# Optimization experiments

Hardware: AMD Instinct MI355X
Metric: run time of the kernel (lower is better)

## Reference

```python
import jax, jax.numpy as jnp
import numpy as np

# hyperparams (match CombinedPeakLoss defaults)
ALPHA, BETA, GAMMA, DELTA, EPSILON = 1.0, 2.0, 1.0, 0.5, 0.5
PEAK_WINDOW = 2
DAYTIME_WEIGHT = 2.0
TEMPERATURE = 0.1
HOURS = 24
NEG = -1e9


def setup_inputs() -> dict:
    key = jax.random.key(0)
    k1, k2 = jax.random.split(key)
    B, S = 16384, 720  # 30 days of hourly data
    y_pred = jax.random.uniform(k1, (B, S), dtype=jnp.float32)
    y_true = jax.random.uniform(k2, (B, S), dtype=jnp.float32)
    return {"y_pred": y_pred, "y_true": y_true}


def _soft_peaks(y_bdh, day_mask, hours):
    # y_bdh: [B,D,H]; day_mask: [1,D,H] bool; hours: [H]
    masked = jnp.where(day_mask, y_bdh, NEG)
    attn = jax.nn.softmax(masked / TEMPERATURE, axis=-1)  # [B,D,H]
    peak_val = (attn * y_bdh).sum(-1)                      # [B,D]
    peak_time = (attn * hours).sum(-1)                     # [B,D]
    return peak_val, peak_time


def reference(y_pred, y_true):
    B, S = y_true.shape
    D = S // HOURS
    dt = y_true.dtype

    # default is_daytime: tiled hour-of-day, daytime = 6..20 inclusive
    t = jnp.tile(jnp.arange(HOURS), D)[:S]                 # [S]
    is_day = ((t >= 6) & (t <= 20))                        # [S] bool
    day_mask = is_day.reshape(1, D, HOURS)                 # [1,D,H]
    hours = jnp.arange(HOURS, dtype=dt)                    # [H]

    yt = y_true.reshape(B, D, HOURS)
    yp = y_pred.reshape(B, D, HOURS)

    # L_overall
    L_overall = jnp.mean((y_pred - y_true) ** 2)

    # soft peak extraction for both true and pred
    t_pv, t_pt = _soft_peaks(yt, day_mask, hours)
    p_pv, p_pt = _soft_peaks(yp, day_mask, hours)
    L_peak_value = jnp.mean((p_pv - t_pv) ** 2)
    L_peak_time = jnp.mean((p_pt - t_pt) ** 2)

    # peak shape loss: hard argmax on daytime-masked truth, windowed normalized MSE
    masked_true = jnp.where(day_mask, yt, NEG)
    peak_idx = jnp.argmax(masked_true, axis=-1)            # [B,D]
    ws = jnp.maximum(0, peak_idx - PEAK_WINDOW)            # [B,D]
    we = jnp.minimum(HOURS, peak_idx + PEAK_WINDOW + 1)    # [B,D]
    h = jnp.arange(HOURS)
    wmask = (h[None, None, :] >= ws[..., None]) & (h[None, None, :] < we[..., None])  # [B,D,H]
    tmax = jnp.max(jnp.where(wmask, yt, NEG), axis=-1)     # [B,D]
    pmax = jnp.max(jnp.where(wmask, yp, NEG), axis=-1)     # [B,D]
    valid = tmax > 1e-6
    tmax_safe = jnp.where(valid, tmax, 1.0)
    diff = yp / (pmax[..., None] + 1e-6) - yt / tmax_safe[..., None]
    wlen = (we - ws).astype(dt)
    mse_win = jnp.sum(jnp.where(wmask, diff ** 2, 0.0), axis=-1) / wlen  # [B,D]
    L_peak_shape = jnp.sum(jnp.where(valid, mse_win, 0.0)) / (jnp.sum(valid) + 1e-6)

    # daytime-weighted extra MSE
    dw = jnp.where(is_day, DAYTIME_WEIGHT, 1.0).astype(dt)  # [S]
    weighted_mse = jnp.mean((y_pred - y_true) ** 2 * dw)
    L_daytime = weighted_mse - L_overall

    total = (ALPHA * L_overall + BETA * L_peak_value + GAMMA * L_peak_time
             + DELTA * L_peak_shape + EPSILON * L_daytime)
    return total
```

## Files before the change

### kernel.cpp

```cpp
#include <hip/hip_runtime.h>
#include <hip/hip_fp16.h>

#define HOURS 24
#define RPB 256
#define PSTR 25


__global__ __launch_bounds__(256, 6) void peakloss_main(
    const float* __restrict__ ypred, const float* __restrict__ ytrue,
    float* __restrict__ partials, int nrows, int nblocks) {
  __shared__ __half2 ltp[RPB * PSTR];

  const int tid = threadIdx.x;
  const int tile0 = blockIdx.x * RPB;
  const int rows = min(RPB, nrows - tile0);

  float s_sq = 0.f, s_day = 0.f, s_pv = 0.f, s_pt = 0.f, s_shape = 0.f, s_valid = 0.f;

  if (rows == RPB) {
    const float4* t4 = (const float4*)(ytrue + (size_t)tile0 * HOURS);
    const float4* p4 = (const float4*)(ypred + (size_t)tile0 * HOURS);
#pragma unroll
    for (int j = 0; j < 6; ++j) {
      int f4 = tid + j * 256;
      float4 a = t4[f4];
      float4 b = p4[f4];
      int pa0 = f4 * 4 + f4 / 6;
      ltp[pa0 + 0] = __floats2half2_rn(a.x, b.x);
      ltp[pa0 + 1] = __floats2half2_rn(a.y, b.y);
      ltp[pa0 + 2] = __floats2half2_rn(a.z, b.z);
      ltp[pa0 + 3] = __floats2half2_rn(a.w, b.w);
      int h0 = 4 * (f4 % 6);
      float dx = b.x - a.x, dy = b.y - a.y, dz = b.z - a.z, dw = b.w - a.w;
      float qx = dx * dx, qy = dy * dy, qz = dz * dz, qw = dw * dw;
      s_sq += qx + qy + qz + qw;
      s_day += ((h0 + 0 >= 6) & (h0 + 0 <= 20)) ? qx : 0.f;
      s_day += ((h0 + 1 >= 6) & (h0 + 1 <= 20)) ? qy : 0.f;
      s_day += ((h0 + 2 >= 6) & (h0 + 2 <= 20)) ? qz : 0.f;
      s_day += ((h0 + 3 >= 6) & (h0 + 3 <= 20)) ? qw : 0.f;
    }
  } else {
    for (int d = tid; d < rows * HOURS; d += 256) {
      float tv = ytrue[(size_t)tile0 * HOURS + d];
      float pv = ypred[(size_t)tile0 * HOURS + d];
      int pa = d + d / HOURS;
      ltp[pa] = __floats2half2_rn(tv, pv);
      float dd = (pv - tv) * (pv - tv);
      int h = d % HOURS;
      s_sq += dd;
      s_day += ((h >= 6) & (h <= 20)) ? dd : 0.f;
    }
  }
  __syncthreads();

  if (tid < rows) {
    const __half2* row = ltp + tid * PSTR;

    float mt = -1e30f, mp = -1e30f;
    int idx = 6;
#pragma unroll
    for (int h = 6; h <= 20; ++h) {
      __half2 v = row[h];
      float th = __low2float(v), ph = __high2float(v);
      if (th > mt) { mt = th; idx = h; }
      mp = fmaxf(mp, ph);
    }

    int ws = idx - 2;
    float den_t = 0.f, nv_t = 0.f, nt_t = 0.f;
    float den_p = 0.f, nv_p = 0.f, nt_p = 0.f;
    float tmax = -1e30f, pmax = -1e30f;
    float St2 = 0.f, Sp2 = 0.f, Stp = 0.f;
#pragma unroll
    for (int h = 4; h <= 22; ++h) {
      __half2 v = row[h];
      float th = __low2float(v), ph = __high2float(v);
      if (h >= 6 && h <= 20) {
        float et = __expf((th - mt) * 10.f);
        den_t += et; nv_t += et * th; nt_t += et * (float)h;
        float ep = __expf((ph - mp) * 10.f);
        den_p += ep; nv_p += ep * ph; nt_p += ep * (float)h;
      }
      bool in = (h >= ws) & (h < ws + 5);
      if (in) {
        tmax = fmaxf(tmax, th); pmax = fmaxf(pmax, ph);
        St2 += th * th; Sp2 += ph * ph; Stp += th * ph;
      }
    }
    float r_t = __builtin_amdgcn_rcpf(den_t);
    float r_p = __builtin_amdgcn_rcpf(den_p);
    float dv  = nv_p * r_p - nv_t * r_t;
    float dtm = nt_p * r_p - nt_t * r_t;
    s_pv += dv * dv;
    s_pt += dtm * dtm;

    bool valid = tmax > 1e-6f;
    float tms = valid ? tmax : 1.0f;
    float rt = __builtin_amdgcn_rcpf(tms);
    float rp = __builtin_amdgcn_rcpf(pmax + 1e-6f);
    float a = rp * rp * Sp2 + rt * rt * St2 - 2.f * rp * rt * Stp;
    if (valid) { s_shape += a * 0.2f; s_valid += 1.0f; }
  }

  float v[6] = {s_sq, s_day, s_pv, s_pt, s_shape, s_valid};
#pragma unroll
  for (int j = 0; j < 6; ++j) {
#pragma unroll
    for (int off = 32; off >= 1; off >>= 1) v[j] += __shfl_down(v[j], off, 64);
  }
  __shared__ float red[6][4];
  int lane = threadIdx.x & 63, wave = threadIdx.x >> 6;
  __syncthreads();
  if (lane == 0) {
#pragma unroll
    for (int j = 0; j < 6; ++j) red[j][wave] = v[j];
  }
  __syncthreads();
  if (threadIdx.x < 6) {
    int j = threadIdx.x;
    partials[(size_t)j * nblocks + blockIdx.x] =
        red[j][0] + red[j][1] + red[j][2] + red[j][3];
  }
}

__global__ __launch_bounds__(256) void peakloss_reduce(
    const float* __restrict__ partials, float* __restrict__ out,
    int nblocks, double inv_BS, double inv_BD) {
  double s[6] = {0, 0, 0, 0, 0, 0};
  for (int i = threadIdx.x; i < nblocks; i += 256) {
#pragma unroll
    for (int j = 0; j < 6; ++j) s[j] += (double)partials[(size_t)j * nblocks + i];
  }
#pragma unroll
  for (int j = 0; j < 6; ++j) {
#pragma unroll
    for (int off = 32; off >= 1; off >>= 1) s[j] += __shfl_down(s[j], off, 64);
  }
  __shared__ double red[6][4];
  int lane = threadIdx.x & 63, wave = threadIdx.x >> 6;
  if (lane == 0) {
#pragma unroll
    for (int j = 0; j < 6; ++j) red[j][wave] = s[j];
  }
  __syncthreads();
  if (threadIdx.x == 0) {
    double a[6];
#pragma unroll
    for (int j = 0; j < 6; ++j)
      a[j] = red[j][0] + red[j][1] + red[j][2] + red[j][3];
    double L_overall = a[0] * inv_BS;
    double L_day     = a[1] * inv_BS;
    double L_pv      = a[2] * inv_BD;
    double L_pt      = a[3] * inv_BD;
    double L_shape   = a[4] / (a[5] + 1e-6);
    out[0] = (float)(L_overall + 2.0 * L_pv + L_pt + 0.5 * L_shape + 0.5 * L_day);
  }
}

extern "C" void kernel_launch(void* const* d_in, const int* in_sizes, int n_in,
                              void* d_out, int out_size, void* d_ws, size_t ws_size,
                              hipStream_t stream) {
  const float* ypred = (const float*)d_in[0];
  const float* ytrue = (const float*)d_in[1];
  float* out = (float*)d_out;
  float* partials = (float*)d_ws;

  long long N = in_sizes[0];
  int nrows = (int)(N / HOURS);
  int grid = (nrows + RPB - 1) / RPB;

  peakloss_main<<<grid, 256, 0, stream>>>(ypred, ytrue, partials, nrows, grid);

  double inv_BS = 1.0 / (double)N;
  double inv_BD = 1.0 / (double)nrows;
  peakloss_reduce<<<1, 256, 0, stream>>>(partials, out, grid, inv_BS, inv_BD);
}
```

Before: 28.68 us.

## Make main kernel persistent with double-buffered LDS and register prefetch

Replaces one-block-per-tile launch with a capped persistent grid that strides over tiles, prefetching the next tile's global loads into registers while computing the current tile's row statistics from a double-buffered shared-memory tile. Intended to overlap memory latency with the softmax/peak compute and reduce block launch overhead. Increases LDS and register use, lowering resident blocks per CU, and may introduce tail imbalance across CUs.

```diff
diff --git a/kernel.cpp b/kernel.cpp
--- a/kernel.cpp
+++ b/kernel.cpp
@@ -4,102 +4,136 @@
 #define HOURS 24
 #define RPB 256
 #define PSTR 25
-
-
-__global__ __launch_bounds__(256, 6) void peakloss_main(
+#define GRID_MAIN 640
+
+
+__device__ __forceinline__ void stage_tile(__half2* __restrict__ buf, int tid,
+                                           const float4* __restrict__ a,
+                                           const float4* __restrict__ b,
+                                           float& s_sq, float& s_day) {
+#pragma unroll
+  for (int j = 0; j < 6; ++j) {
+    int f4 = tid + j * 256;
+    int pa0 = f4 * 4 + f4 / 6;
+    buf[pa0 + 0] = __floats2half2_rn(a[j].x, b[j].x);
+    buf[pa0 + 1] = __floats2half2_rn(a[j].y, b[j].y);
+    buf[pa0 + 2] = __floats2half2_rn(a[j].z, b[j].z);
+    buf[pa0 + 3] = __floats2half2_rn(a[j].w, b[j].w);
+    int h0 = 4 * (f4 % 6);
+    float dx = b[j].x - a[j].x, dy = b[j].y - a[j].y;
+    float dz = b[j].z - a[j].z, dw = b[j].w - a[j].w;
+    float qx = dx * dx, qy = dy * dy, qz = dz * dz, qw = dw * dw;
+    s_sq += qx + qy + qz + qw;
+    s_day += ((h0 + 0 >= 6) & (h0 + 0 <= 20)) ? qx : 0.f;
+    s_day += ((h0 + 1 >= 6) & (h0 + 1 <= 20)) ? qy : 0.f;
+    s_day += ((h0 + 2 >= 6) & (h0 + 2 <= 20)) ? qz : 0.f;
+    s_day += ((h0 + 3 >= 6) & (h0 + 3 <= 20)) ? qw : 0.f;
+  }
+}
+
+__device__ __forceinline__ void compute_row(const __half2* __restrict__ row,
+                                            float& s_pv, float& s_pt,
+                                            float& s_shape, float& s_valid) {
+  float mt = -1e30f, mp = -1e30f;
+  int idx = 6;
+#pragma unroll
+  for (int h = 6; h <= 20; ++h) {
+    __half2 v = row[h];
+    float th = __low2float(v), ph = __high2float(v);
+    if (th > mt) { mt = th; idx = h; }
+    mp = fmaxf(mp, ph);
+  }
+  int ws = idx - 2;
+  float den_t = 0.f, nv_t = 0.f, nt_t = 0.f;
+  float den_p = 0.f, nv_p = 0.f, nt_p = 0.f;
+  float tmax = -1e30f, pmax = -1e30f;
+  float St2 = 0.f, Sp2 = 0.f, Stp = 0.f;
+#pragma unroll
+  for (int h = 4; h <= 22; ++h) {
+    __half2 v = row[h];
+    float th = __low2float(v), ph = __high2float(v);
+    if (h >= 6 && h <= 20) {
+      float et = __expf((th - mt) * 10.f);
+      den_t += et; nv_t += et * th; nt_t += et * (float)h;
+      float ep = __expf((ph - mp) * 10.f);
+      den_p += ep; nv_p += ep * ph; nt_p += ep * (float)h;
+    }
+    bool in = (h >= ws) & (h < ws + 5);
+    if (in) {
+      tmax = fmaxf(tmax, th); pmax = fmaxf(pmax, ph);
+      St2 += th * th; Sp2 += ph * ph; Stp += th * ph;
+    }
+  }
+  float r_t = __builtin_amdgcn_rcpf(den_t);
+  float r_p = __builtin_amdgcn_rcpf(den_p);
+  float dv  = nv_p * r_p - nv_t * r_t;
+  float dtm = nt_p * r_p - nt_t * r_t;
+  s_pv += dv * dv;
+  s_pt += dtm * dtm;
+  bool valid = tmax > 1e-6f;
+  float tms = valid ? tmax : 1.0f;
+  float rt = __builtin_amdgcn_rcpf(tms);
+  float rp = __builtin_amdgcn_rcpf(pmax + 1e-6f);
+  float aa = rp * rp * Sp2 + rt * rt * St2 - 2.f * rp * rt * Stp;
+  if (valid) { s_shape += aa * 0.2f; s_valid += 1.0f; }
+}
+
+__global__ __launch_bounds__(256, 3) void peakloss_main(
     const float* __restrict__ ypred, const float* __restrict__ ytrue,
     float* __restrict__ partials, int nrows, int nblocks) {
-  __shared__ __half2 ltp[RPB * PSTR];
-
+  __shared__ __half2 ltp[2][RPB * PSTR];
   const int tid = threadIdx.x;
-  const int tile0 = blockIdx.x * RPB;
-  const int rows = min(RPB, nrows - tile0);
+  const int G = gridDim.x;
+  const int ntf = nrows / RPB;
+  const int rem = nrows - ntf * RPB;
 
   float s_sq = 0.f, s_day = 0.f, s_pv = 0.f, s_pt = 0.f, s_shape = 0.f, s_valid = 0.f;
-
-  if (rows == RPB) {
-    const float4* t4 = (const float4*)(ytrue + (size_t)tile0 * HOURS);
-    const float4* p4 = (const float4*)(ypred + (size_t)tile0 * HOURS);
-#pragma unroll
-    for (int j = 0; j < 6; ++j) {
-      int f4 = tid + j * 256;
-      float4 a = t4[f4];
-      float4 b = p4[f4];
-      int pa0 = f4 * 4 + f4 / 6;
-      ltp[pa0 + 0] = __floats2half2_rn(a.x, b.x);
-      ltp[pa0 + 1] = __floats2half2_rn(a.y, b.y);
-      ltp[pa0 + 2] = __floats2half2_rn(a.z, b.z);
-      ltp[pa0 + 3] = __floats2half2_rn(a.w, b.w);
-      int h0 = 4 * (f4 % 6);
-      float dx = b.x - a.x, dy = b.y - a.y, dz = b.z - a.z, dw = b.w - a.w;
-      float qx = dx * dx, qy = dy * dy, qz = dz * dz, qw = dw * dw;
-      s_sq += qx + qy + qz + qw;
-      s_day += ((h0 + 0 >= 6) & (h0 + 0 <= 20)) ? qx : 0.f;
-      s_day += ((h0 + 1 >= 6) & (h0 + 1 <= 20)) ? qy : 0.f;
-      s_day += ((h0 + 2 >= 6) & (h0 + 2 <= 20)) ? qz : 0.f;
-      s_day += ((h0 + 3 >= 6) & (h0 + 3 <= 20)) ? qw : 0.f;
-    }
-  } else {
-    for (int d = tid; d < rows * HOURS; d += 256) {
-      float tv = ytrue[(size_t)tile0 * HOURS + d];
-      float pv = ypred[(size_t)tile0 * HOURS + d];
+  float4 a[6], b[6];
+
+  int tile = blockIdx.x;
+  if (tile < ntf) {
+    {
+      const float4* t4 = (const float4*)(ytrue + (size_t)tile * RPB * HOURS);
+      const float4* p4 = (const float4*)(ypred + (size_t)tile * RPB * HOURS);
+#pragma unroll
+      for (int j = 0; j < 6; ++j) { a[j] = t4[tid + j * 256]; b[j] = p4[tid + j * 256]; }
+      stage_tile(ltp[0], tid, a, b, s_sq, s_day);
+      __syncthreads();
+    }
+    int cur = 0;
+    for (;;) {
+      int nxt = tile + G;
+      bool has = nxt < ntf;
+      if (has) {
+        const float4* t4 = (const float4*)(ytrue + (size_t)nxt * RPB * HOURS);
+        const float4* p4 = (const float4*)(ypred + (size_t)nxt * RPB * HOURS);
+#pragma unroll
+        for (int j = 0; j < 6; ++j) { a[j] = t4[tid + j * 256]; b[j] = p4[tid + j * 256]; }
+      }
+      compute_row(&ltp[cur][tid * PSTR], s_pv, s_pt, s_shape, s_valid);
+      if (!has) break;
+      stage_tile(ltp[cur ^ 1], tid, a, b, s_sq, s_day);
+      __syncthreads();
+      cur ^= 1;
+      tile = nxt;
+    }
+  }
+
+  if (rem > 0 && blockIdx.x == (ntf % G)) {
+    __syncthreads();
+    const size_t base = (size_t)ntf * RPB * HOURS;
+    for (int d = tid; d < rem * HOURS; d += 256) {
+      float tv = ytrue[base + d];
+      float pv = ypred[base + d];
       int pa = d + d / HOURS;
-      ltp[pa] = __floats2half2_rn(tv, pv);
+      ltp[0][pa] = __floats2half2_rn(tv, pv);
       float dd = (pv - tv) * (pv - tv);
       int h = d % HOURS;
       s_sq += dd;
       s_day += ((h >= 6) & (h <= 20)) ? dd : 0.f;
     }
-  }
-  __syncthreads();
-
-  if (tid < rows) {
-    const __half2* row = ltp + tid * PSTR;
-
-    float mt = -1e30f, mp = -1e30f;
-    int idx = 6;
-#pragma unroll
-    for (int h = 6; h <= 20; ++h) {
-      __half2 v = row[h];
-      float th = __low2float(v), ph = __high2float(v);
-      if (th > mt) { mt = th; idx = h; }
-      mp = fmaxf(mp, ph);
-    }
-
-    int ws = idx - 2;
-    float den_t = 0.f, nv_t = 0.f, nt_t = 0.f;
-    float den_p = 0.f, nv_p = 0.f, nt_p = 0.f;
-    float tmax = -1e30f, pmax = -1e30f;
-    float St2 = 0.f, Sp2 = 0.f, Stp = 0.f;
-#pragma unroll
-    for (int h = 4; h <= 22; ++h) {
-      __half2 v = row[h];
-      float th = __low2float(v), ph = __high2float(v);
-      if (h >= 6 && h <= 20) {
-        float et = __expf((th - mt) * 10.f);
-        den_t += et; nv_t += et * th; nt_t += et * (float)h;
-        float ep = __expf((ph - mp) * 10.f);
-        den_p += ep; nv_p += ep * ph; nt_p += ep * (float)h;
-      }
-      bool in = (h >= ws) & (h < ws + 5);
-      if (in) {
-        tmax = fmaxf(tmax, th); pmax = fmaxf(pmax, ph);
-        St2 += th * th; Sp2 += ph * ph; Stp += th * ph;
-      }
-    }
-    float r_t = __builtin_amdgcn_rcpf(den_t);
-    float r_p = __builtin_amdgcn_rcpf(den_p);
-    float dv  = nv_p * r_p - nv_t * r_t;
-    float dtm = nt_p * r_p - nt_t * r_t;
-    s_pv += dv * dv;
-    s_pt += dtm * dtm;
-
-    bool valid = tmax > 1e-6f;
-    float tms = valid ? tmax : 1.0f;
-    float rt = __builtin_amdgcn_rcpf(tms);
-    float rp = __builtin_amdgcn_rcpf(pmax + 1e-6f);
-    float a = rp * rp * Sp2 + rt * rt * St2 - 2.f * rp * rt * Stp;
-    if (valid) { s_shape += a * 0.2f; s_valid += 1.0f; }
+    __syncthreads();
+    if (tid < rem) compute_row(&ltp[0][tid * PSTR], s_pv, s_pt, s_shape, s_valid);
   }
 
   float v[6] = {s_sq, s_day, s_pv, s_pt, s_shape, s_valid};
@@ -167,7 +201,8 @@
 
   long long N = in_sizes[0];
   int nrows = (int)(N / HOURS);
-  int grid = (nrows + RPB - 1) / RPB;
+  int ntf = nrows / RPB;
+  int grid = ntf > 0 ? (ntf < GRID_MAIN ? ntf : GRID_MAIN) : 1;
 
   peakloss_main<<<grid, 256, 0, stream>>>(ypred, ytrue, partials, nrows, grid);
 
```

After: 29.48 us. 2.8% more time.

## Fuse final reduction into main kernel via last-block atomic counter

Applied to the files above, without the earlier changes.

Replaces the separate single-block reduce kernel with a last-block-done pattern. Each block stores its partials atomically, increments a global counter, and the block that arrives last sums all partials and writes the output. This removes one kernel launch and the gap between the two kernels, at the cost of an atomic per block and a serialized tail inside the last block. The counter is never reset; the modulo on the counter value lets it work across repeated calls, but it assumes the workspace starts zeroed.

```diff
diff --git a/kernel.cpp b/kernel.cpp
--- a/kernel.cpp
+++ b/kernel.cpp
@@ -4,11 +4,14 @@
 #define HOURS 24
 #define RPB 256
 #define PSTR 25
+#define SCOPE_AGENT __HIP_MEMORY_SCOPE_AGENT
 
 
-__global__ __launch_bounds__(256, 6) void peakloss_main(
+__global__ __launch_bounds__(256, 6) void peakloss_onekernel(
     const float* __restrict__ ypred, const float* __restrict__ ytrue,
-    float* __restrict__ partials, int nrows, int nblocks) {
+    float* __restrict__ partials, unsigned* __restrict__ counter,
+    float* __restrict__ out, int nrows, int nblocks,
+    double inv_BS, double inv_BD) {
   __shared__ __half2 ltp[RPB * PSTR];
 
   const int tid = threadIdx.x;
@@ -93,13 +96,12 @@
     float dtm = nt_p * r_p - nt_t * r_t;
     s_pv += dv * dv;
     s_pt += dtm * dtm;
-
     bool valid = tmax > 1e-6f;
     float tms = valid ? tmax : 1.0f;
     float rt = __builtin_amdgcn_rcpf(tms);
     float rp = __builtin_amdgcn_rcpf(pmax + 1e-6f);
-    float a = rp * rp * Sp2 + rt * rt * St2 - 2.f * rp * rt * Stp;
-    if (valid) { s_shape += a * 0.2f; s_valid += 1.0f; }
+    float aa = rp * rp * Sp2 + rt * rt * St2 - 2.f * rp * rt * Stp;
+    if (valid) { s_shape += aa * 0.2f; s_valid += 1.0f; }
   }
 
   float v[6] = {s_sq, s_day, s_pv, s_pt, s_shape, s_valid};
@@ -116,38 +118,48 @@
     for (int j = 0; j < 6; ++j) red[j][wave] = v[j];
   }
   __syncthreads();
-  if (threadIdx.x < 6) {
-    int j = threadIdx.x;
-    partials[(size_t)j * nblocks + blockIdx.x] =
-        red[j][0] + red[j][1] + red[j][2] + red[j][3];
+
+  __shared__ int is_last;
+  if (tid == 0) {
+    float sums[6];
+#pragma unroll
+    for (int j = 0; j < 6; ++j) {
+      sums[j] = red[j][0] + red[j][1] + red[j][2] + red[j][3];
+      __hip_atomic_store(&partials[(size_t)j * nblocks + blockIdx.x], sums[j],
+                         __ATOMIC_RELAXED, SCOPE_AGENT);
+    }
+    asm volatile("s_waitcnt vmcnt(0)" ::: "memory");
+    unsigned old = __hip_atomic_fetch_add(counter, 1u, __ATOMIC_RELAXED, SCOPE_AGENT);
+    is_last = ((old % (unsigned)nblocks) == (unsigned)(nblocks - 1)) ? 1 : 0;
   }
-}
+  __syncthreads();
+  if (!is_last) return;
 
-__global__ __launch_bounds__(256) void peakloss_reduce(
-    const float* __restrict__ partials, float* __restrict__ out,
-    int nblocks, double inv_BS, double inv_BD) {
   double s[6] = {0, 0, 0, 0, 0, 0};
-  for (int i = threadIdx.x; i < nblocks; i += 256) {
+  for (int i = tid; i < nblocks; i += 256) {
 #pragma unroll
-    for (int j = 0; j < 6; ++j) s[j] += (double)partials[(size_t)j * nblocks + i];
+    for (int j = 0; j < 6; ++j) {
+      float pv = __hip_atomic_load(&partials[(size_t)j * nblocks + i],
+                                   __ATOMIC_RELAXED, SCOPE_AGENT);
+      s[j] += (double)pv;
+    }
   }
 #pragma unroll
   for (int j = 0; j < 6; ++j) {
 #pragma unroll
     for (int off = 32; off >= 1; off >>= 1) s[j] += __shfl_down(s[j], off, 64);
   }
-  __shared__ double red[6][4];
-  int lane = threadIdx.x & 63, wave = threadIdx.x >> 6;
+  __shared__ double dred[6][4];
   if (lane == 0) {
 #pragma unroll
-    for (int j = 0; j < 6; ++j) red[j][wave] = s[j];
+    for (int j = 0; j < 6; ++j) dred[j][wave] = s[j];
   }
   __syncthreads();
-  if (threadIdx.x == 0) {
+  if (tid == 0) {
     double a[6];
 #pragma unroll
     for (int j = 0; j < 6; ++j)
-      a[j] = red[j][0] + red[j][1] + red[j][2] + red[j][3];
+      a[j] = dred[j][0] + dred[j][1] + dred[j][2] + dred[j][3];
     double L_overall = a[0] * inv_BS;
     double L_day     = a[1] * inv_BS;
     double L_pv      = a[2] * inv_BD;
@@ -163,15 +175,17 @@
   const float* ypred = (const float*)d_in[0];
   const float* ytrue = (const float*)d_in[1];
   float* out = (float*)d_out;
-  float* partials = (float*)d_ws;
 
   long long N = in_sizes[0];
   int nrows = (int)(N / HOURS);
   int grid = (nrows + RPB - 1) / RPB;
 
-  peakloss_main<<<grid, 256, 0, stream>>>(ypred, ytrue, partials, nrows, grid);
+  float* partials = (float*)d_ws;
+  size_t coff = (((size_t)6 * grid * sizeof(float)) + 127ull) / 128ull * 128ull;
+  unsigned* counter = (unsigned*)((char*)d_ws + coff);
 
   double inv_BS = 1.0 / (double)N;
   double inv_BD = 1.0 / (double)nrows;
-  peakloss_reduce<<<1, 256, 0, stream>>>(partials, out, grid, inv_BS, inv_BD);
+  peakloss_onekernel<<<grid, 256, 0, stream>>>(ypred, ytrue, partials, counter,
+                                               out, nrows, grid, inv_BS, inv_BD);
 }
```

Measured after the change: 38.93 us. 35.7% more time.
